# Kernel tuning notes

Hardware: AMD Instinct MI355X
Metric: run time of the kernel (lower is better)

Reference implementation:

```python
import math
import jax, jax.numpy as jnp
import numpy as np

LMAX = 2


def _cg_complex(j1, m1, j2, m2, j3, m3):
    # Standard (Racah) Clebsch-Gordan coefficient <j1 m1 j2 m2 | j3 m3> for integer l.
    if m1 + m2 != m3 or j3 < abs(j1 - j2) or j3 > j1 + j2:
        return 0.0
    f = math.factorial
    pre = math.sqrt((2 * j3 + 1) * f(j3 + j1 - j2) * f(j3 - j1 + j2) * f(j1 + j2 - j3) / f(j1 + j2 + j3 + 1))
    pre *= math.sqrt(f(j3 + m3) * f(j3 - m3) * f(j1 - m1) * f(j1 + m1) * f(j2 - m2) * f(j2 + m2))
    kmin = max(0, j2 - j3 - m1, j1 + m2 - j3)
    kmax = min(j1 + j2 - j3, j1 - m1, j2 + m2)
    s = 0.0
    for k in range(kmin, kmax + 1):
        s += (-1.0) ** k / (f(k) * f(j1 + j2 - j3 - k) * f(j1 - m1 - k) * f(j2 + m2 - k) * f(j3 - j2 + m1 + k) * f(j3 - j1 - m2 + k))
    return pre * s


def _u_matrix(l):
    # Unitary map from complex SH (Condon-Shortley) to real SH, rows = real mu, cols = complex m.
    U = np.zeros((2 * l + 1, 2 * l + 1), dtype=np.complex128)
    U[l, l] = 1.0
    isq2 = 1.0 / math.sqrt(2.0)
    for m in range(1, l + 1):
        U[l + m, l - m] = isq2
        U[l + m, l + m] = ((-1.0) ** m) * isq2
        U[l - m, l - m] = 1j * isq2
        U[l - m, l + m] = -1j * ((-1.0) ** m) * isq2
    return U


def _real_clebsch_gordan(lmax):
    # Dense real-SH CG tensor over combined s=(l,m) indices, shape [S,S,S], S=(lmax+1)^2.
    S = (lmax + 1) ** 2
    cg = np.zeros((S, S, S))
    for l1 in range(lmax + 1):
        for l2 in range(lmax + 1):
            for l3 in range(abs(l1 - l2), min(lmax, l1 + l2) + 1):
                blk = np.zeros((2 * l1 + 1, 2 * l2 + 1, 2 * l3 + 1))
                for i1, m1 in enumerate(range(-l1, l1 + 1)):
                    for i2, m2 in enumerate(range(-l2, l2 + 1)):
                        for i3, m3 in enumerate(range(-l3, l3 + 1)):
                            blk[i1, i2, i3] = _cg_complex(l1, m1, l2, m2, l3, m3)
                U1, U2, U3 = _u_matrix(l1), _u_matrix(l2), _u_matrix(l3)
                r = np.einsum('am,bn,co,mno->abc', U1, U2, U3.conj(), blk.astype(np.complex128))
                r = r.real if (l1 + l2 + l3) % 2 == 0 else r.imag  # parity-dependent real part
                cg[l1 * l1:(l1 + 1) ** 2, l2 * l2:(l2 + 1) ** 2, l3 * l3:(l3 + 1) ** 2] = r
    return cg


def _sparse_cg(lmax):
    cg = _real_clebsch_gordan(lmax)
    i1, i2, i3 = np.nonzero(np.abs(cg) > 1e-10)
    vals = cg[i1, i2, i3].astype(np.float32)
    widx = np.floor(np.sqrt(i3.astype(np.float64))).astype(np.int32)  # l of output combined index
    return vals, i1.astype(np.int32), i2.astype(np.int32), i3.astype(np.int32), widx


def _spherical_harmonics_l2(d):
    # Real SH up to l=2, 'component' normalization (|x|=1 assumed). Order: (l,m) = (0,0),(1,-1),(1,0),(1,1),(2,-2..2).
    x, y, z = d[..., 0], d[..., 1], d[..., 2]
    s3, s5, s15 = math.sqrt(3.0), math.sqrt(5.0), math.sqrt(15.0)
    return jnp.stack([
        jnp.ones_like(x),
        s3 * y, s3 * z, s3 * x,
        s15 * x * y, s15 * y * z, 0.5 * s5 * (3.0 * z * z - 1.0), s15 * x * z, 0.5 * s15 * (x * x - y * y),
    ], axis=-1)


def setup_inputs():
    N_ATOMS, N_EDGES, N_BASIS, N_RADIAL = 1200, 12000, 128, 20
    S = (LMAX + 1) ** 2
    key = jax.random.key(0)
    ks = jax.random.split(key, 8)
    vals, i1, i2, i3, widx = _sparse_cg(LMAX)
    return {
        'x': jax.random.normal(ks[0], (N_ATOMS, S, N_BASIS), jnp.float32),
        'radial_ij': jax.random.uniform(ks[1], (N_EDGES, N_RADIAL), jnp.float32),
        'dir_ij': jax.random.normal(ks[2], (N_EDGES, 3), jnp.float32),
        'cutoff_ij': jax.random.uniform(ks[3], (N_EDGES, 1), jnp.float32),
        'W_filter': jax.random.normal(ks[6], (N_RADIAL, N_BASIS * (LMAX + 1)), jnp.float32) / math.sqrt(N_RADIAL),
        'b_filter': jnp.zeros((N_BASIS * (LMAX + 1),), jnp.float32),
        'cg_vals': jnp.asarray(vals),
        'idx_i': jax.random.randint(ks[4], (N_EDGES,), 0, N_ATOMS),
        'idx_j': jax.random.randint(ks[5], (N_EDGES,), 0, N_ATOMS),
        'cg_idx_in1': jnp.asarray(i1),
        'cg_idx_in2': jnp.asarray(i2),
        'cg_idx_out': jnp.asarray(i3),
        'w_idx': jnp.asarray(widx),
    }


def reference(x, radial_ij, dir_ij, cutoff_ij, W_filter, b_filter, cg_vals,
              idx_i, idx_j, cg_idx_in1, cg_idx_in2, cg_idx_out, w_idx):
    n_atoms, S, F = x.shape
    E = dir_ij.shape[0]
    d = dir_ij / jnp.linalg.norm(dir_ij, axis=-1, keepdims=True)
    Y = _spherical_harmonics_l2(d)                        # [E, S]
    Wij = (radial_ij @ W_filter + b_filter) * cutoff_ij   # [E, (lmax+1)*F]
    Wij = Wij.reshape(E, LMAX + 1, F)                     # per-l radial filter
    xj = x[idx_j]                                         # [E, S, F] neighbor features
    # Sparse CG tensor-product contraction over combined (l,m) indices.
    v = (Y[:, cg_idx_in2, None] * cg_vals[None, :, None]
         * Wij[:, w_idx, :] * xj[:, cg_idx_in1, :])       # [E, n_cg, F]
    yij = jnp.zeros((E, S, F), v.dtype).at[:, cg_idx_out, :].add(v)
    return jax.ops.segment_sum(yij, idx_i, num_segments=n_atoms)
```

## Files before the change

### kernel.cpp

```cpp
#include <hip/hip_runtime.h>
#include <math.h>


#define S9      9
#define NF      128
#define NRAD    20
#define MAXDEG  64
#define MSTRIDE 96

__device__ inline float2 f2fma(float a, float2 b, float2 c) {
    return make_float2(fmaf(a, b.x, c.x), fmaf(a, b.y, c.y));
}

__global__ __launch_bounds__(64) void prep_kernel(
    const float* __restrict__ radial,
    const float* __restrict__ dir,
    const float* __restrict__ cutoff,
    const float* __restrict__ Wf,
    const float* __restrict__ bf,
    const float* __restrict__ cg_vals,
    const int* __restrict__ idx_i,
    const int* __restrict__ cg_i1,
    const int* __restrict__ cg_i2,
    const int* __restrict__ cg_i3,
    int ncg,
    int* __restrict__ cnt,
    int* __restrict__ elist,
    float* __restrict__ Mall,
    float* __restrict__ Wij)
{
    const int e = blockIdx.x;
    const int t = threadIdx.x;

    __shared__ float Msh[81];
    __shared__ float Ysh[9];

    if (t < 81) Msh[t] = 0.0f;
    if (t + 64 < 81) Msh[t + 64] = 0.0f;

    if (t == 0) {
        float dx = dir[3 * e], dy = dir[3 * e + 1], dz = dir[3 * e + 2];
        const float inv = rsqrtf(dx * dx + dy * dy + dz * dz);
        dx *= inv; dy *= inv; dz *= inv;
        const float s3c  = 1.7320508075688772f;
        const float s5c  = 2.2360679774997896f;
        const float s15c = 3.8729833462074170f;
        Ysh[0] = 1.0f;
        Ysh[1] = s3c * dy;
        Ysh[2] = s3c * dz;
        Ysh[3] = s3c * dx;
        Ysh[4] = s15c * dx * dy;
        Ysh[5] = s15c * dy * dz;
        Ysh[6] = 0.5f * s5c * (3.0f * dz * dz - 1.0f);
        Ysh[7] = s15c * dx * dz;
        Ysh[8] = 0.5f * s15c * (dx * dx - dy * dy);
        const int i = idx_i[e];
        const int pos = atomicAdd(&cnt[i], 1);
        if (pos < MAXDEG) elist[i * MAXDEG + pos] = e;
    }
    __syncthreads();

    for (int k = t; k < ncg; k += 64)
        atomicAdd(&Msh[cg_i1[k] * S9 + cg_i3[k]], cg_vals[k] * Ysh[cg_i2[k]]);

    float rad[NRAD];
    #pragma unroll
    for (int r = 0; r < NRAD; ++r) rad[r] = radial[e * NRAD + r];
    const float cut = cutoff[e];

    float2 w0 = ((const float2*)(bf + 0 * NF))[t];
    float2 w1 = ((const float2*)(bf + 1 * NF))[t];
    float2 w2 = ((const float2*)(bf + 2 * NF))[t];
    #pragma unroll
    for (int r = 0; r < NRAD; ++r) {
        const float2* row = (const float2*)(Wf + r * (3 * NF));
        w0 = f2fma(rad[r], row[t],       w0);
        w1 = f2fma(rad[r], row[t + 64],  w1);
        w2 = f2fma(rad[r], row[t + 128], w2);
    }
    w0.x *= cut; w0.y *= cut;
    w1.x *= cut; w1.y *= cut;
    w2.x *= cut; w2.y *= cut;

    float2* wp = (float2*)(Wij + (size_t)e * (3 * NF));
    wp[t]       = w0;
    wp[t + 64]  = w1;
    wp[t + 128] = w2;

    __syncthreads();
    float* mp = Mall + (size_t)e * MSTRIDE;
    if (t < 81) mp[t] = Msh[t];
    if (t + 64 < 81) mp[t + 64] = Msh[t + 64];
}

__global__ __launch_bounds__(256) void atom_kernel(
    const float* __restrict__ x,
    const float* __restrict__ Mall,
    const float* __restrict__ Wij,
    const int* __restrict__ cnt,
    const int* __restrict__ elist,
    const int* __restrict__ idx_j,
    float* __restrict__ out)
{
    const int a = blockIdx.x;
    const int tid = threadIdx.x;
    const int w = tid >> 6;
    const int t = tid & 63;
    const int deg = min(cnt[a], MAXDEG);
    const int* el = elist + a * MAXDEG;

    __shared__ float sacc[4][S9][NF];

    float2 acc[S9];
    #pragma unroll
    for (int s = 0; s < S9; ++s) acc[s] = make_float2(0.f, 0.f);

    int k = w;
    int e_cur = 0, j_cur = 0;
    if (k < deg) {
        e_cur = __builtin_amdgcn_readfirstlane(el[k]);
        j_cur = __builtin_amdgcn_readfirstlane(idx_j[e_cur]);
    }
    while (k < deg) {
        const int kn = k + 4;
        int e_nx = 0, j_nx = 0;
        if (kn < deg) {
            e_nx = __builtin_amdgcn_readfirstlane(el[kn]);
            j_nx = __builtin_amdgcn_readfirstlane(idx_j[e_nx]);
        }

        const float*  Me = Mall + (size_t)e_cur * MSTRIDE;
        const float2* xp = (const float2*)(x + (size_t)j_cur * (S9 * NF)) + t;
        const float2* wp = (const float2*)(Wij + (size_t)e_cur * (3 * NF)) + t;

        float2 xj[S9];
        #pragma unroll
        for (int s = 0; s < S9; ++s) xj[s] = xp[s * 64];
        const float2 wl0 = wp[0];
        const float2 wl1 = wp[64];
        const float2 wl2 = wp[128];

        float2 ts[S9];
        #pragma unroll
        for (int s3 = 0; s3 < S9; ++s3)
            ts[s3] = make_float2(Me[s3] * xj[0].x, Me[s3] * xj[0].y);
        #pragma unroll
        for (int s1 = 1; s1 < S9; ++s1) {
            #pragma unroll
            for (int s3 = 0; s3 < S9; ++s3)
                ts[s3] = f2fma(Me[s1 * S9 + s3], xj[s1], ts[s3]);
        }
        #pragma unroll
        for (int s3 = 0; s3 < S9; ++s3) {
            const float2 ww = (s3 == 0) ? wl0 : ((s3 < 4) ? wl1 : wl2);
            acc[s3].x = fmaf(ww.x, ts[s3].x, acc[s3].x);
            acc[s3].y = fmaf(ww.y, ts[s3].y, acc[s3].y);
        }

        k = kn; e_cur = e_nx; j_cur = j_nx;
    }

    #pragma unroll
    for (int s = 0; s < S9; ++s)
        *(float2*)&sacc[w][s][2 * t] = acc[s];
    __syncthreads();

    for (int idx = tid; idx < S9 * 64; idx += 256) {
        const int s  = idx >> 6;
        const int tp = idx & 63;
        float2 v0 = *(const float2*)&sacc[0][s][2 * tp];
        float2 v1 = *(const float2*)&sacc[1][s][2 * tp];
        float2 v2 = *(const float2*)&sacc[2][s][2 * tp];
        float2 v3 = *(const float2*)&sacc[3][s][2 * tp];
        float2 r = make_float2((v0.x + v1.x) + (v2.x + v3.x),
                               (v0.y + v1.y) + (v2.y + v3.y));
        *(float2*)&out[(size_t)a * (S9 * NF) + s * NF + 2 * tp] = r;
    }
}

extern "C" void kernel_launch(void* const* d_in, const int* in_sizes, int n_in,
                              void* d_out, int out_size, void* d_ws, size_t ws_size,
                              hipStream_t stream) {
    const float* x       = (const float*)d_in[0];
    const float* radial  = (const float*)d_in[1];
    const float* dir     = (const float*)d_in[2];
    const float* cutoff  = (const float*)d_in[3];
    const float* Wf      = (const float*)d_in[4];
    const float* bf      = (const float*)d_in[5];
    const float* cg_vals = (const float*)d_in[6];
    const int*   idx_i   = (const int*)d_in[7];
    const int*   idx_j   = (const int*)d_in[8];
    const int*   cg_i1   = (const int*)d_in[9];
    const int*   cg_i2   = (const int*)d_in[10];
    const int*   cg_i3   = (const int*)d_in[11];

    const int E   = in_sizes[7];
    const int ncg = in_sizes[6];
    const int A   = in_sizes[0] / (S9 * NF);

    int* cnt   = (int*)d_ws;
    int* elist = cnt + A;
    size_t off = ((size_t)(A + A * MAXDEG) * sizeof(int) + 511) & ~(size_t)511;
    float* Mall = (float*)((char*)d_ws + off);
    float* Wij  = Mall + (size_t)E * MSTRIDE;

    hipMemsetAsync(cnt, 0, (size_t)A * sizeof(int), stream);

    prep_kernel<<<E, 64, 0, stream>>>(
        radial, dir, cutoff, Wf, bf, cg_vals, idx_i,
        cg_i1, cg_i2, cg_i3, ncg, cnt, elist, Mall, Wij);

    atom_kernel<<<A, 256, 0, stream>>>(
        x, Mall, Wij, cnt, elist, idx_j, (float*)d_out);
}
```

Before: 131.5 us.

## Fuse per-edge filter and CG matrix computation into atom kernel

Removes the per-edge prep kernel, which wrote a CG-contracted 9x9 matrix and a radial filter per edge to global memory. Each wavefront in the atom kernel now recomputes the spherical harmonics, the 9x9 matrix (via LDS atomics) and the radial filter on the fly, and a tiny kernel only builds the per-atom edge lists. This trades global memory round trips and a large grid launch for extra per-edge compute and LDS traffic inside the atom loop. It also relies on wave-synchronous LDS use with only block-level fences instead of barriers, and drops the software prefetch of the next edge indices.

```diff
diff --git a/kernel.cpp b/kernel.cpp
--- a/kernel.cpp
+++ b/kernel.cpp
@@ -2,153 +2,139 @@
 #include <math.h>
 
 
-#define S9      9
-#define NF      128
-#define NRAD    20
-#define MAXDEG  64
-#define MSTRIDE 96
+#define S9     9
+#define NF     128
+#define NRAD   20
+#define MAXDEG 64
+#define MPAD   12
 
 __device__ inline float2 f2fma(float a, float2 b, float2 c) {
     return make_float2(fmaf(a, b.x, c.x), fmaf(a, b.y, c.y));
 }
 
-__global__ __launch_bounds__(64) void prep_kernel(
+__global__ void build_kernel(const int* __restrict__ idx_i, int E,
+                             int* __restrict__ cnt, int* __restrict__ elist) {
+    int e = blockIdx.x * blockDim.x + threadIdx.x;
+    if (e < E) {
+        int i = idx_i[e];
+        int pos = atomicAdd(&cnt[i], 1);
+        if (pos < MAXDEG) elist[i * MAXDEG + pos] = e;
+    }
+}
+
+__global__ __launch_bounds__(256, 4) void atom_kernel(
+    const float* __restrict__ x,
     const float* __restrict__ radial,
     const float* __restrict__ dir,
     const float* __restrict__ cutoff,
     const float* __restrict__ Wf,
     const float* __restrict__ bf,
     const float* __restrict__ cg_vals,
-    const int* __restrict__ idx_i,
+    const int* __restrict__ idx_j,
     const int* __restrict__ cg_i1,
     const int* __restrict__ cg_i2,
     const int* __restrict__ cg_i3,
     int ncg,
-    int* __restrict__ cnt,
-    int* __restrict__ elist,
-    float* __restrict__ Mall,
-    float* __restrict__ Wij)
-{
-    const int e = blockIdx.x;
-    const int t = threadIdx.x;
-
-    __shared__ float Msh[81];
-    __shared__ float Ysh[9];
-
-    if (t < 81) Msh[t] = 0.0f;
-    if (t + 64 < 81) Msh[t + 64] = 0.0f;
-
-    if (t == 0) {
-        float dx = dir[3 * e], dy = dir[3 * e + 1], dz = dir[3 * e + 2];
-        const float inv = rsqrtf(dx * dx + dy * dy + dz * dz);
-        dx *= inv; dy *= inv; dz *= inv;
-        const float s3c  = 1.7320508075688772f;
-        const float s5c  = 2.2360679774997896f;
-        const float s15c = 3.8729833462074170f;
-        Ysh[0] = 1.0f;
-        Ysh[1] = s3c * dy;
-        Ysh[2] = s3c * dz;
-        Ysh[3] = s3c * dx;
-        Ysh[4] = s15c * dx * dy;
-        Ysh[5] = s15c * dy * dz;
-        Ysh[6] = 0.5f * s5c * (3.0f * dz * dz - 1.0f);
-        Ysh[7] = s15c * dx * dz;
-        Ysh[8] = 0.5f * s15c * (dx * dx - dy * dy);
-        const int i = idx_i[e];
-        const int pos = atomicAdd(&cnt[i], 1);
-        if (pos < MAXDEG) elist[i * MAXDEG + pos] = e;
-    }
-    __syncthreads();
-
-    for (int k = t; k < ncg; k += 64)
-        atomicAdd(&Msh[cg_i1[k] * S9 + cg_i3[k]], cg_vals[k] * Ysh[cg_i2[k]]);
-
-    float rad[NRAD];
-    #pragma unroll
-    for (int r = 0; r < NRAD; ++r) rad[r] = radial[e * NRAD + r];
-    const float cut = cutoff[e];
-
-    float2 w0 = ((const float2*)(bf + 0 * NF))[t];
-    float2 w1 = ((const float2*)(bf + 1 * NF))[t];
-    float2 w2 = ((const float2*)(bf + 2 * NF))[t];
-    #pragma unroll
-    for (int r = 0; r < NRAD; ++r) {
-        const float2* row = (const float2*)(Wf + r * (3 * NF));
-        w0 = f2fma(rad[r], row[t],       w0);
-        w1 = f2fma(rad[r], row[t + 64],  w1);
-        w2 = f2fma(rad[r], row[t + 128], w2);
-    }
-    w0.x *= cut; w0.y *= cut;
-    w1.x *= cut; w1.y *= cut;
-    w2.x *= cut; w2.y *= cut;
-
-    float2* wp = (float2*)(Wij + (size_t)e * (3 * NF));
-    wp[t]       = w0;
-    wp[t + 64]  = w1;
-    wp[t + 128] = w2;
-
-    __syncthreads();
-    float* mp = Mall + (size_t)e * MSTRIDE;
-    if (t < 81) mp[t] = Msh[t];
-    if (t + 64 < 81) mp[t + 64] = Msh[t + 64];
-}
-
-__global__ __launch_bounds__(256) void atom_kernel(
-    const float* __restrict__ x,
-    const float* __restrict__ Mall,
-    const float* __restrict__ Wij,
     const int* __restrict__ cnt,
     const int* __restrict__ elist,
-    const int* __restrict__ idx_j,
     float* __restrict__ out)
 {
-    const int a = blockIdx.x;
+    const int a   = blockIdx.x;
     const int tid = threadIdx.x;
-    const int w = tid >> 6;
-    const int t = tid & 63;
+    const int w   = tid >> 6;
+    const int t   = tid & 63;
     const int deg = min(cnt[a], MAXDEG);
-    const int* el = elist + a * MAXDEG;
 
     __shared__ float sacc[4][S9][NF];
+    __shared__ __align__(16) float Msh[4][S9 * MPAD];
+    __shared__ __align__(16) float Ysh[4][12];
+
+    int  adr1 = 0, iy1 = 0, adr2 = 0, iy2 = 0;
+    float cv1 = 0.f, cv2 = 0.f;
+    const bool has1 = (t < ncg);
+    const bool has2 = (t + 64 < ncg);
+    if (has1) { adr1 = cg_i1[t] * MPAD + cg_i3[t];           iy1 = cg_i2[t];      cv1 = cg_vals[t]; }
+    if (has2) { adr2 = cg_i1[t + 64] * MPAD + cg_i3[t + 64]; iy2 = cg_i2[t + 64]; cv2 = cg_vals[t + 64]; }
+    const bool more = (ncg > 128);
+
+    const float2 b0 = ((const float2*)(bf + 0 * NF))[t];
+    const float2 b1 = ((const float2*)(bf + 1 * NF))[t];
+    const float2 b2 = ((const float2*)(bf + 2 * NF))[t];
 
     float2 acc[S9];
     #pragma unroll
     for (int s = 0; s < S9; ++s) acc[s] = make_float2(0.f, 0.f);
 
-    int k = w;
-    int e_cur = 0, j_cur = 0;
-    if (k < deg) {
-        e_cur = __builtin_amdgcn_readfirstlane(el[k]);
-        j_cur = __builtin_amdgcn_readfirstlane(idx_j[e_cur]);
-    }
-    while (k < deg) {
-        const int kn = k + 4;
-        int e_nx = 0, j_nx = 0;
-        if (kn < deg) {
-            e_nx = __builtin_amdgcn_readfirstlane(el[kn]);
-            j_nx = __builtin_amdgcn_readfirstlane(idx_j[e_nx]);
+    float* Mw = Msh[w];
+    float* Yw = Ysh[w];
+
+    for (int k = w; k < deg; k += 4) {
+        const int e = __builtin_amdgcn_readfirstlane(elist[a * MAXDEG + k]);
+        const int j = __builtin_amdgcn_readfirstlane(idx_j[e]);
+
+        if (t < 54) ((float2*)Mw)[t] = make_float2(0.f, 0.f);
+
+        {
+            float dx = dir[3 * e], dy = dir[3 * e + 1], dz = dir[3 * e + 2];
+            const float inv = rsqrtf(dx * dx + dy * dy + dz * dz);
+            dx *= inv; dy *= inv; dz *= inv;
+            const float s3c  = 1.7320508075688772f;
+            const float s5c  = 2.2360679774997896f;
+            const float s15c = 3.8729833462074170f;
+            if (t == 0) {
+                *(float4*)&Yw[0] = make_float4(1.0f, s3c * dy, s3c * dz, s3c * dx);
+                *(float4*)&Yw[4] = make_float4(s15c * dx * dy, s15c * dy * dz,
+                                               0.5f * s5c * (3.0f * dz * dz - 1.0f),
+                                               s15c * dx * dz);
+                Yw[8] = 0.5f * s15c * (dx * dx - dy * dy);
+            }
         }
+        __threadfence_block();
 
-        const float*  Me = Mall + (size_t)e_cur * MSTRIDE;
-        const float2* xp = (const float2*)(x + (size_t)j_cur * (S9 * NF)) + t;
-        const float2* wp = (const float2*)(Wij + (size_t)e_cur * (3 * NF)) + t;
+        if (has1) atomicAdd(&Mw[adr1], cv1 * Yw[iy1]);
+        if (has2) atomicAdd(&Mw[adr2], cv2 * Yw[iy2]);
+        if (more) {
+            for (int kk = t + 128; kk < ncg; kk += 64)
+                atomicAdd(&Mw[cg_i1[kk] * MPAD + cg_i3[kk]], cg_vals[kk] * Yw[cg_i2[kk]]);
+        }
+        __threadfence_block();
 
+        const float cut = cutoff[e];
+        float2 wl0 = b0, wl1 = b1, wl2 = b2;
+        #pragma unroll
+        for (int r = 0; r < NRAD; ++r) {
+            const float rr = radial[e * NRAD + r];
+            const float2* row = (const float2*)(Wf + r * (3 * NF));
+            wl0 = f2fma(rr, row[t],       wl0);
+            wl1 = f2fma(rr, row[t + 64],  wl1);
+            wl2 = f2fma(rr, row[t + 128], wl2);
+        }
+        wl0.x *= cut; wl0.y *= cut;
+        wl1.x *= cut; wl1.y *= cut;
+        wl2.x *= cut; wl2.y *= cut;
+
+        const float2* xp = (const float2*)(x + (size_t)j * (S9 * NF)) + t;
         float2 xj[S9];
         #pragma unroll
         for (int s = 0; s < S9; ++s) xj[s] = xp[s * 64];
-        const float2 wl0 = wp[0];
-        const float2 wl1 = wp[64];
-        const float2 wl2 = wp[128];
 
         float2 ts[S9];
         #pragma unroll
-        for (int s3 = 0; s3 < S9; ++s3)
-            ts[s3] = make_float2(Me[s3] * xj[0].x, Me[s3] * xj[0].y);
+        for (int s = 0; s < S9; ++s) ts[s] = make_float2(0.f, 0.f);
         #pragma unroll
-        for (int s1 = 1; s1 < S9; ++s1) {
-            #pragma unroll
-            for (int s3 = 0; s3 < S9; ++s3)
-                ts[s3] = f2fma(Me[s1 * S9 + s3], xj[s1], ts[s3]);
+        for (int s1 = 0; s1 < S9; ++s1) {
+            const float4 m0 = *(const float4*)&Mw[s1 * MPAD];
+            const float4 m1 = *(const float4*)&Mw[s1 * MPAD + 4];
+            const float  m8 = Mw[s1 * MPAD + 8];
+            ts[0] = f2fma(m0.x, xj[s1], ts[0]);
+            ts[1] = f2fma(m0.y, xj[s1], ts[1]);
+            ts[2] = f2fma(m0.z, xj[s1], ts[2]);
+            ts[3] = f2fma(m0.w, xj[s1], ts[3]);
+            ts[4] = f2fma(m1.x, xj[s1], ts[4]);
+            ts[5] = f2fma(m1.y, xj[s1], ts[5]);
+            ts[6] = f2fma(m1.z, xj[s1], ts[6]);
+            ts[7] = f2fma(m1.w, xj[s1], ts[7]);
+            ts[8] = f2fma(m8,   xj[s1], ts[8]);
         }
         #pragma unroll
         for (int s3 = 0; s3 < S9; ++s3) {
@@ -156,8 +142,7 @@
             acc[s3].x = fmaf(ww.x, ts[s3].x, acc[s3].x);
             acc[s3].y = fmaf(ww.y, ts[s3].y, acc[s3].y);
         }
-
-        k = kn; e_cur = e_nx; j_cur = j_nx;
+        __threadfence_block();
     }
 
     #pragma unroll
@@ -200,16 +185,12 @@
 
     int* cnt   = (int*)d_ws;
     int* elist = cnt + A;
-    size_t off = ((size_t)(A + A * MAXDEG) * sizeof(int) + 511) & ~(size_t)511;
-    float* Mall = (float*)((char*)d_ws + off);
-    float* Wij  = Mall + (size_t)E * MSTRIDE;
 
     hipMemsetAsync(cnt, 0, (size_t)A * sizeof(int), stream);
 
-    prep_kernel<<<E, 64, 0, stream>>>(
-        radial, dir, cutoff, Wf, bf, cg_vals, idx_i,
-        cg_i1, cg_i2, cg_i3, ncg, cnt, elist, Mall, Wij);
+    build_kernel<<<(E + 255) / 256, 256, 0, stream>>>(idx_i, E, cnt, elist);
 
     atom_kernel<<<A, 256, 0, stream>>>(
-        x, Mall, Wij, cnt, elist, idx_j, (float*)d_out);
+        x, radial, dir, cutoff, Wf, bf, cg_vals,
+        idx_j, cg_i1, cg_i2, cg_i3, ncg, cnt, elist, (float*)d_out);
 }
```

After: 201.8 us. 1.54x slower.

## Compute radial filter weights inside atom kernel instead of via workspace

Applied to the files above, without the earlier changes.

Moves the per-edge radial filter matmul (radial @ W_filter + bias, times cutoff) out of the prep kernel and recomputes it on the fly inside the atom gather loop. This removes the per-edge Wij write and reread through global memory (E x 384 floats each way). In exchange, each edge iteration in the atom kernel now does 20 extra loads of W_filter rows (likely cache-resident) and 60 FMAs per lane, which lengthens the dependent chain per edge.

```diff
diff --git a/kernel.cpp b/kernel.cpp
--- a/kernel.cpp
+++ b/kernel.cpp
@@ -13,11 +13,7 @@
 }
 
 __global__ __launch_bounds__(64) void prep_kernel(
-    const float* __restrict__ radial,
     const float* __restrict__ dir,
-    const float* __restrict__ cutoff,
-    const float* __restrict__ Wf,
-    const float* __restrict__ bf,
     const float* __restrict__ cg_vals,
     const int* __restrict__ idx_i,
     const int* __restrict__ cg_i1,
@@ -26,8 +22,7 @@
     int ncg,
     int* __restrict__ cnt,
     int* __restrict__ elist,
-    float* __restrict__ Mall,
-    float* __restrict__ Wij)
+    float* __restrict__ Mall)
 {
     const int e = blockIdx.x;
     const int t = threadIdx.x;
@@ -62,32 +57,8 @@
 
     for (int k = t; k < ncg; k += 64)
         atomicAdd(&Msh[cg_i1[k] * S9 + cg_i3[k]], cg_vals[k] * Ysh[cg_i2[k]]);
+    __syncthreads();
 
-    float rad[NRAD];
-    #pragma unroll
-    for (int r = 0; r < NRAD; ++r) rad[r] = radial[e * NRAD + r];
-    const float cut = cutoff[e];
-
-    float2 w0 = ((const float2*)(bf + 0 * NF))[t];
-    float2 w1 = ((const float2*)(bf + 1 * NF))[t];
-    float2 w2 = ((const float2*)(bf + 2 * NF))[t];
-    #pragma unroll
-    for (int r = 0; r < NRAD; ++r) {
-        const float2* row = (const float2*)(Wf + r * (3 * NF));
-        w0 = f2fma(rad[r], row[t],       w0);
-        w1 = f2fma(rad[r], row[t + 64],  w1);
-        w2 = f2fma(rad[r], row[t + 128], w2);
-    }
-    w0.x *= cut; w0.y *= cut;
-    w1.x *= cut; w1.y *= cut;
-    w2.x *= cut; w2.y *= cut;
-
-    float2* wp = (float2*)(Wij + (size_t)e * (3 * NF));
-    wp[t]       = w0;
-    wp[t + 64]  = w1;
-    wp[t + 128] = w2;
-
-    __syncthreads();
     float* mp = Mall + (size_t)e * MSTRIDE;
     if (t < 81) mp[t] = Msh[t];
     if (t + 64 < 81) mp[t + 64] = Msh[t + 64];
@@ -95,21 +66,27 @@
 
 __global__ __launch_bounds__(256) void atom_kernel(
     const float* __restrict__ x,
-    const float* __restrict__ Mall,
-    const float* __restrict__ Wij,
+    const float* __restrict__ radial,
+    const float* __restrict__ cutoff,
+    const float* __restrict__ Wf,
+    const float* __restrict__ bf,
+    const int* __restrict__ idx_j,
     const int* __restrict__ cnt,
     const int* __restrict__ elist,
-    const int* __restrict__ idx_j,
+    const float* __restrict__ Mall,
     float* __restrict__ out)
 {
-    const int a = blockIdx.x;
+    const int a   = blockIdx.x;
     const int tid = threadIdx.x;
-    const int w = tid >> 6;
-    const int t = tid & 63;
+    const int w   = tid >> 6;
+    const int t   = tid & 63;
     const int deg = min(cnt[a], MAXDEG);
-    const int* el = elist + a * MAXDEG;
 
     __shared__ float sacc[4][S9][NF];
+
+    const float2 b0 = ((const float2*)(bf + 0 * NF))[t];
+    const float2 b1 = ((const float2*)(bf + 1 * NF))[t];
+    const float2 b2 = ((const float2*)(bf + 2 * NF))[t];
 
     float2 acc[S9];
     #pragma unroll
@@ -118,34 +95,43 @@
     int k = w;
     int e_cur = 0, j_cur = 0;
     if (k < deg) {
-        e_cur = __builtin_amdgcn_readfirstlane(el[k]);
+        e_cur = __builtin_amdgcn_readfirstlane(elist[a * MAXDEG + k]);
         j_cur = __builtin_amdgcn_readfirstlane(idx_j[e_cur]);
     }
     while (k < deg) {
         const int kn = k + 4;
         int e_nx = 0, j_nx = 0;
         if (kn < deg) {
-            e_nx = __builtin_amdgcn_readfirstlane(el[kn]);
+            e_nx = __builtin_amdgcn_readfirstlane(elist[a * MAXDEG + kn]);
             j_nx = __builtin_amdgcn_readfirstlane(idx_j[e_nx]);
         }
 
-        const float*  Me = Mall + (size_t)e_cur * MSTRIDE;
         const float2* xp = (const float2*)(x + (size_t)j_cur * (S9 * NF)) + t;
-        const float2* wp = (const float2*)(Wij + (size_t)e_cur * (3 * NF)) + t;
-
         float2 xj[S9];
         #pragma unroll
         for (int s = 0; s < S9; ++s) xj[s] = xp[s * 64];
-        const float2 wl0 = wp[0];
-        const float2 wl1 = wp[64];
-        const float2 wl2 = wp[128];
 
+        const float* rp = radial + (size_t)e_cur * NRAD;
+        const float cut = cutoff[e_cur];
+        float2 wl0 = b0, wl1 = b1, wl2 = b2;
+        #pragma unroll
+        for (int r = 0; r < NRAD; ++r) {
+            const float rr = rp[r];
+            const float2* row = (const float2*)(Wf + r * (3 * NF));
+            wl0 = f2fma(rr, row[t],       wl0);
+            wl1 = f2fma(rr, row[t + 64],  wl1);
+            wl2 = f2fma(rr, row[t + 128], wl2);
+        }
+        wl0.x *= cut; wl0.y *= cut;
+        wl1.x *= cut; wl1.y *= cut;
+        wl2.x *= cut; wl2.y *= cut;
+
+        const float* Me = Mall + (size_t)e_cur * MSTRIDE;
         float2 ts[S9];
         #pragma unroll
-        for (int s3 = 0; s3 < S9; ++s3)
-            ts[s3] = make_float2(Me[s3] * xj[0].x, Me[s3] * xj[0].y);
+        for (int s = 0; s < S9; ++s) ts[s] = make_float2(0.f, 0.f);
         #pragma unroll
-        for (int s1 = 1; s1 < S9; ++s1) {
+        for (int s1 = 0; s1 < S9; ++s1) {
             #pragma unroll
             for (int s3 = 0; s3 < S9; ++s3)
                 ts[s3] = f2fma(Me[s1 * S9 + s3], xj[s1], ts[s3]);
@@ -202,14 +188,12 @@
     int* elist = cnt + A;
     size_t off = ((size_t)(A + A * MAXDEG) * sizeof(int) + 511) & ~(size_t)511;
     float* Mall = (float*)((char*)d_ws + off);
-    float* Wij  = Mall + (size_t)E * MSTRIDE;
 
     hipMemsetAsync(cnt, 0, (size_t)A * sizeof(int), stream);
 
     prep_kernel<<<E, 64, 0, stream>>>(
-        radial, dir, cutoff, Wf, bf, cg_vals, idx_i,
-        cg_i1, cg_i2, cg_i3, ncg, cnt, elist, Mall, Wij);
+        dir, cg_vals, idx_i, cg_i1, cg_i2, cg_i3, ncg, cnt, elist, Mall);
 
     atom_kernel<<<A, 256, 0, stream>>>(
-        x, Mall, Wij, cnt, elist, idx_j, (float*)d_out);
+        x, radial, cutoff, Wf, bf, idx_j, cnt, elist, Mall, (float*)d_out);
 }
```

Result: slower. 163.4 us (+24.3%).
